# Optimization experiments

Measured on AMD Instinct MI355X. Metric: run time of the kernel, lower is better.

The kernel has to match this reference:

```python
import jax, jax.numpy as jnp
import numpy as np

N_HEADS = 4
N_HIDDEN = 64  # out_features // n_heads
NEG_SLOPE = 0.2


def setup_inputs() -> dict:
    key = jax.random.key(0)
    k1, k2, k3, k4, k5 = jax.random.split(key, 5)
    B, N, F_IN, F_OUT = 1, 4096, 128, 256
    h = jax.random.normal(k1, (B, N, F_IN), dtype=jnp.float32)
    adj_mat = jax.random.uniform(k2, (N, N, 1), dtype=jnp.float32)
    W_proj = jax.random.normal(k3, (F_IN, N_HEADS * N_HIDDEN), dtype=jnp.float32) / np.sqrt(F_IN)
    W_proj_attn = jax.random.normal(k4, (F_IN, N_HEADS * N_HIDDEN // 2), dtype=jnp.float32) / np.sqrt(F_IN)
    w_attn = jax.random.normal(k5, (N_HIDDEN,), dtype=jnp.float32) / np.sqrt(N_HIDDEN)
    return {"h": h, "adj_mat": adj_mat, "W_proj": W_proj, "W_proj_attn": W_proj_attn, "w_attn": w_attn}


def reference(h, adj_mat, W_proj, W_proj_attn, w_attn):
    B, N, _ = h.shape
    H, D = N_HEADS, N_HIDDEN
    half = D // 2
    # value projection: (B, N, H, D)
    g = (h @ W_proj).reshape(B, N, H, D)
    # attention-feature projection: (B, N, H, D//2)
    ga = (h @ W_proj_attn).reshape(B, N, H, half)
    # attn(cat([ga_i, ga_j])) decomposes linearly: e_ij = <w_l, ga_i> + <w_r, ga_j>
    # (identical math to the torch repeat/cat/Linear, without the NxNxD tensor)
    el = jnp.einsum('bnhk,k->bnh', ga, w_attn[:half])   # dest node i term
    er = jnp.einsum('bnhk,k->bnh', ga, w_attn[half:])   # source node j term
    e = jax.nn.leaky_relu(el[:, :, None, :] + er[:, None, :, :], NEG_SLOPE)  # (B, N, N, H)
    mask = adj_mat >= 0.5  # (N, N, 1) broadcasts over (B, N, N, H)
    e = jnp.where(mask, e, -jnp.inf)
    a = jax.nn.softmax(e, axis=2)  # softmax over source nodes j
    # dropout is identity in eval mode
    out = jnp.einsum('bijh,bjhf->bihf', a, g)  # (B, N, H, D)
    return out.reshape(B, N, H * D)  # is_concat=True
```

## Files before the change

### kernel.cpp

```cpp
#include <hip/hip_runtime.h>
#include <hip/hip_bf16.h>

typedef __bf16 bf16_t;
typedef __bf16 bf16x4 __attribute__((ext_vector_type(4)));
typedef __bf16 bf16x8 __attribute__((ext_vector_type(8)));
typedef float floatx4 __attribute__((ext_vector_type(4)));
typedef unsigned int u32;

#define N_NODES 4096
#define F_IN 128
#define NUM_HEADS 4
#define D_HID 64
#define F_OUT 256
#define NEG_SLOPE 0.2f
#define LOG2E 1.4426950408889634f
#define NWORDS 128

__global__ __launch_bounds__(256) void mask_kernel(
    const float* __restrict__ adj, u32* __restrict__ maskT)
{
    const int w = blockIdx.x * 256 + threadIdx.x;
    const float* src = adj + (size_t)w * 32;
    u32 bits = 0;
#pragma unroll
    for (int c = 0; c < 8; ++c) {
        const float4 v = *reinterpret_cast<const float4*>(src + c * 4);
        bits |= (u32)(v.x >= 0.5f) << (4 * c + 0);
        bits |= (u32)(v.y >= 0.5f) << (4 * c + 1);
        bits |= (u32)(v.z >= 0.5f) << (4 * c + 2);
        bits |= (u32)(v.w >= 0.5f) << (4 * c + 3);
    }
    const int row = w >> 7;
    const int jw  = w & 127;
    maskT[(size_t)jw * N_NODES + row] = bits;
}

__global__ __launch_bounds__(384) void proj_kernel(
    const float* __restrict__ hmat, const float* __restrict__ Wp,
    const float* __restrict__ Wa, const float* __restrict__ wattn,
    bf16_t* __restrict__ GB, float* __restrict__ el, float* __restrict__ er)
{
    const int t = threadIdx.x;
    const int j0 = blockIdx.x * 8;

    float acc[8] = {0.f, 0.f, 0.f, 0.f, 0.f, 0.f, 0.f, 0.f};

    const float* wptr;
    int stride;
    if (t < 256) { wptr = Wp + t;         stride = 256; }
    else         { wptr = Wa + (t - 256); stride = 128; }

    const float* hbase = hmat + (size_t)j0 * F_IN;

    for (int m = 0; m < F_IN; m += 4) {
        const float w0 = wptr[(size_t)(m + 0) * stride];
        const float w1 = wptr[(size_t)(m + 1) * stride];
        const float w2 = wptr[(size_t)(m + 2) * stride];
        const float w3 = wptr[(size_t)(m + 3) * stride];
#pragma unroll
        for (int jl = 0; jl < 8; ++jl) {
            const float4 hv = *reinterpret_cast<const float4*>(&hbase[jl * F_IN + m]);
            acc[jl] = fmaf(hv.w, w3, fmaf(hv.z, w2, fmaf(hv.y, w1, fmaf(hv.x, w0, acc[jl]))));
        }
    }

    if (t < 256) {
        const int h = t >> 6, f = t & 63;
        bf16x8 o;
#pragma unroll
        for (int q = 0; q < 8; ++q) o[q] = (bf16_t)acc[q];
        const size_t base = ((((size_t)h * 128 + (j0 >> 5)) * 4 + (f >> 4)) * 64
                             + (f & 15) + 16 * ((j0 >> 3) & 3)) * 8;
        *reinterpret_cast<bf16x8*>(&GB[base]) = o;
    } else {
        const int ta = t - 256;
        const int ha = ta >> 5, k = ta & 31;
        const float wl = wattn[k] * LOG2E, wr = wattn[32 + k] * LOG2E;
#pragma unroll
        for (int jl = 0; jl < 8; ++jl) {
            float vl = acc[jl] * wl;
            float vr = acc[jl] * wr;
#pragma unroll
            for (int s = 16; s >= 1; s >>= 1) {
                vl += __shfl_xor(vl, s, 64);
                vr += __shfl_xor(vr, s, 64);
            }
            if (k == 0) {
                el[ha * N_NODES + j0 + jl] = vl;
                er[ha * N_NODES + j0 + jl] = vr;
            }
        }
    }
}

__global__ __launch_bounds__(256, 4) void attn_kernel(
    const u32* __restrict__ maskT, const bf16_t* __restrict__ GB,
    const float* __restrict__ el, const float* __restrict__ er,
    float* __restrict__ numout, float* __restrict__ den_g,
    int ntiles)
{
    const int tid  = threadIdx.x;
    const int wave = tid >> 6;
    const int i0   = blockIdx.x * 128 + wave * 32;
    const int jc   = blockIdx.y;
    const int hh   = blockIdx.z;
    const int lane = tid & 63;
    const int m    = lane & 15;
    const int quad = lane >> 4;
    const int NS   = ntiles * 2;
    const int j32_0 = jc * NS;

    const float el_lo = el[hh * N_NODES + i0 + m];
    const float el_hi = el[hh * N_NODES + i0 + 16 + m];
    const u32*  mTp   = maskT + (size_t)j32_0 * N_NODES + i0 + m;
    const float* erp  = er + hh * N_NODES + j32_0 * 32 + quad * 8;
    const bf16_t* gb  = GB + (size_t)hh * (128 * 4 * 512)
                           + (size_t)j32_0 * 2048 + lane * 8;

    floatx4 accL0 = {0.f, 0.f, 0.f, 0.f};
    floatx4 accL1 = accL0, accL2 = accL0, accL3 = accL0;
    floatx4 accH0 = accL0, accH1 = accL0, accH2 = accL0, accH3 = accL0;
    float denL = 0.f, denH = 0.f;

    u32 mLc = mTp[0], mHc = mTp[16];
    float4 e0c = *reinterpret_cast<const float4*>(erp);
    float4 e1c = *reinterpret_cast<const float4*>(erp + 4);
    bf16x8 b0c = *reinterpret_cast<const bf16x8*>(gb);
    bf16x8 b1c = *reinterpret_cast<const bf16x8*>(gb + 512);
    bf16x8 b2c = *reinterpret_cast<const bf16x8*>(gb + 1024);
    bf16x8 b3c = *reinterpret_cast<const bf16x8*>(gb + 1536);

    for (int s = 0; s < NS; ++s) {
        const int d = (s + 1 < NS) ? 1 : 0;
        const u32    mLn = mTp[(size_t)d * N_NODES];
        const u32    mHn = mTp[(size_t)d * N_NODES + 16];
        const float4 e0n = *reinterpret_cast<const float4*>(erp + d * 32);
        const float4 e1n = *reinterpret_cast<const float4*>(erp + d * 32 + 4);
        const bf16_t* gpn = gb + (size_t)d * 2048;
        const bf16x8 b0n = *reinterpret_cast<const bf16x8*>(gpn);
        const bf16x8 b1n = *reinterpret_cast<const bf16x8*>(gpn + 512);
        const bf16x8 b2n = *reinterpret_cast<const bf16x8*>(gpn + 1024);
        const bf16x8 b3n = *reinterpret_cast<const bf16x8*>(gpn + 1536);

        const u32 byL = (mLc >> (quad * 8)) & 0xffu;
        const u32 byH = (mHc >> (quad * 8)) & 0xffu;
        const float ev[8] = {e0c.x, e0c.y, e0c.z, e0c.w, e1c.x, e1c.y, e1c.z, e1c.w};

        bf16x8 afL, afH;
        float dL = 0.f, dH = 0.f;
#pragma unroll
        for (int q = 0; q < 8; ++q) {
            float sL = el_lo + ev[q]; sL = fmaxf(sL, NEG_SLOPE * sL);
            float sH = el_hi + ev[q]; sH = fmaxf(sH, NEG_SLOPE * sH);
            const float pL = ((byL >> q) & 1u) ? __builtin_amdgcn_exp2f(sL) : 0.f;
            const float pH = ((byH >> q) & 1u) ? __builtin_amdgcn_exp2f(sH) : 0.f;
            dL += pL; dH += pH;
            afL[q] = (bf16_t)pL;
            afH[q] = (bf16_t)pH;
        }
        denL += dL; denH += dH;

        accL0 = __builtin_amdgcn_mfma_f32_16x16x32_bf16(afL, b0c, accL0, 0, 0, 0);
        accH0 = __builtin_amdgcn_mfma_f32_16x16x32_bf16(afH, b0c, accH0, 0, 0, 0);
        accL1 = __builtin_amdgcn_mfma_f32_16x16x32_bf16(afL, b1c, accL1, 0, 0, 0);
        accH1 = __builtin_amdgcn_mfma_f32_16x16x32_bf16(afH, b1c, accH1, 0, 0, 0);
        accL2 = __builtin_amdgcn_mfma_f32_16x16x32_bf16(afL, b2c, accL2, 0, 0, 0);
        accH2 = __builtin_amdgcn_mfma_f32_16x16x32_bf16(afH, b2c, accH2, 0, 0, 0);
        accL3 = __builtin_amdgcn_mfma_f32_16x16x32_bf16(afL, b3c, accL3, 0, 0, 0);
        accH3 = __builtin_amdgcn_mfma_f32_16x16x32_bf16(afH, b3c, accH3, 0, 0, 0);

        mLc = mLn; mHc = mHn; e0c = e0n; e1c = e1n;
        b0c = b0n; b1c = b1n; b2c = b2n; b3c = b3n;
        mTp += N_NODES;
        erp += 32;
        gb  += 2048;
    }

    denL += __shfl_xor(denL, 16, 64);
    denL += __shfl_xor(denL, 32, 64);
    denH += __shfl_xor(denH, 16, 64);
    denH += __shfl_xor(denH, 32, 64);

    float* nrow = numout + (size_t)jc * ((size_t)N_NODES * F_OUT);
    const int ibL = i0 + quad * 4;
    const int ibH = ibL + 16;
#pragma unroll
    for (int r = 0; r < 4; ++r) {
        float* dL = nrow + (size_t)(ibL + r) * F_OUT + hh * D_HID + m;
        dL[0]  = accL0[r];
        dL[16] = accL1[r];
        dL[32] = accL2[r];
        dL[48] = accL3[r];
        float* dH = nrow + (size_t)(ibH + r) * F_OUT + hh * D_HID + m;
        dH[0]  = accH0[r];
        dH[16] = accH1[r];
        dH[32] = accH2[r];
        dH[48] = accH3[r];
    }
    if (quad == 0) {
        den_g[((size_t)jc * N_NODES + i0 + m) * NUM_HEADS + hh] = denL;
        den_g[((size_t)jc * N_NODES + i0 + 16 + m) * NUM_HEADS + hh] = denH;
    }
}

template<int NJC>
__global__ __launch_bounds__(256) void reduce_kernel(
    const float* __restrict__ num, const float* __restrict__ den,
    float* __restrict__ out)
{
    const int t4   = blockIdx.x * 256 + threadIdx.x;
    const int base = t4 * 4;
    const int i  = base >> 8;
    const int hh = (base & 255) >> 6;
    float4 n = {0.f, 0.f, 0.f, 0.f};
    float d = 0.f;
#pragma unroll
    for (int jc = 0; jc < NJC; ++jc) {
        const float4 v = *reinterpret_cast<const float4*>(
            num + (size_t)jc * ((size_t)N_NODES * F_OUT) + base);
        n.x += v.x; n.y += v.y; n.z += v.z; n.w += v.w;
        d += den[((size_t)jc * N_NODES + i) * NUM_HEADS + hh];
    }
    const float rd = 1.0f / d;
    float4 o = {n.x * rd, n.y * rd, n.z * rd, n.w * rd};
    *reinterpret_cast<float4*>(out + base) = o;
}

extern "C" void kernel_launch(void* const* d_in, const int* in_sizes, int n_in,
                              void* d_out, int out_size, void* d_ws, size_t ws_size,
                              hipStream_t stream)
{
    const float* hmat = (const float*)d_in[0];
    const float* adj  = (const float*)d_in[1];
    const float* Wp   = (const float*)d_in[2];
    const float* Wa   = (const float*)d_in[3];
    const float* watt = (const float*)d_in[4];
    float* out = (float*)d_out;

    char* ws = (char*)d_ws;
    bf16_t* GB   = (bf16_t*)ws;
    float*  el   = (float*)(ws + (2ull << 20));
    float*  er   = (float*)(ws + (2ull << 20) + (64ull << 10));
    u32*    mskT = (u32*)(ws + (2ull << 20) + (128ull << 10));
    const size_t baseoff = (4ull << 20) + (128ull << 10);

    const size_t num_bytes = (size_t)N_NODES * F_OUT * 4;
    const size_t den_bytes = (size_t)N_NODES * NUM_HEADS * 4;
    const int njc = (ws_size >= baseoff + 8 * (num_bytes + den_bytes)) ? 8
                  : (ws_size >= baseoff + 4 * (num_bytes + den_bytes)) ? 4 : 2;

    float* num = (float*)(ws + baseoff);
    float* den = (float*)(ws + baseoff + (size_t)njc * num_bytes);

    proj_kernel<<<512, 384, 0, stream>>>(hmat, Wp, Wa, watt, GB, el, er);
    mask_kernel<<<(N_NODES * NWORDS) / 256, 256, 0, stream>>>(adj, mskT);
    attn_kernel<<<dim3(32, njc, NUM_HEADS), 256, 0, stream>>>(
        mskT, GB, el, er, num, den, (N_NODES / njc) / 64);
    if (njc == 8)      reduce_kernel<8><<<(N_NODES * F_OUT) / 1024, 256, 0, stream>>>(num, den, out);
    else if (njc == 4) reduce_kernel<4><<<(N_NODES * F_OUT) / 1024, 256, 0, stream>>>(num, den, out);
    else               reduce_kernel<2><<<(N_NODES * F_OUT) / 1024, 256, 0, stream>>>(num, den, out);
}
```

Measured before the change: 166.2 us.

## Fuse mask and projection kernels; compute softmax denominators via MFMA with ones

Merges the adjacency bit-packing kernel and the projection kernel into one launch, with the block index choosing which role a block plays. This removes one kernel launch and lets the two independent jobs run on the GPU at the same time. The attention loop now gets row sums by multiplying the bf16 probabilities by a ones vector on the matrix cores, which replaces the scalar float adds and cross-lane shuffles. It also packs the leaky-relu arithmetic into float2 vectors. The cost is two extra MFMAs per step, and the denominators are now summed from bf16-rounded probabilities, which slightly changes numerics.

```diff
diff --git a/kernel.cpp b/kernel.cpp
--- a/kernel.cpp
+++ b/kernel.cpp
@@ -4,6 +4,7 @@
 typedef __bf16 bf16_t;
 typedef __bf16 bf16x4 __attribute__((ext_vector_type(4)));
 typedef __bf16 bf16x8 __attribute__((ext_vector_type(8)));
+typedef float floatx2 __attribute__((ext_vector_type(2)));
 typedef float floatx4 __attribute__((ext_vector_type(4)));
 typedef unsigned int u32;
 
@@ -15,33 +16,36 @@
 #define NEG_SLOPE 0.2f
 #define LOG2E 1.4426950408889634f
 #define NWORDS 128
-
-__global__ __launch_bounds__(256) void mask_kernel(
-    const float* __restrict__ adj, u32* __restrict__ maskT)
-{
-    const int w = blockIdx.x * 256 + threadIdx.x;
-    const float* src = adj + (size_t)w * 32;
-    u32 bits = 0;
-#pragma unroll
-    for (int c = 0; c < 8; ++c) {
-        const float4 v = *reinterpret_cast<const float4*>(src + c * 4);
-        bits |= (u32)(v.x >= 0.5f) << (4 * c + 0);
-        bits |= (u32)(v.y >= 0.5f) << (4 * c + 1);
-        bits |= (u32)(v.z >= 0.5f) << (4 * c + 2);
-        bits |= (u32)(v.w >= 0.5f) << (4 * c + 3);
-    }
-    const int row = w >> 7;
-    const int jw  = w & 127;
-    maskT[(size_t)jw * N_NODES + row] = bits;
-}
-
-__global__ __launch_bounds__(384) void proj_kernel(
+#define MASK_BLOCKS 1366
+#define PROJ_BLOCKS 512
+
+__global__ __launch_bounds__(384) void prep_kernel(
+    const float* __restrict__ adj, u32* __restrict__ maskT,
     const float* __restrict__ hmat, const float* __restrict__ Wp,
     const float* __restrict__ Wa, const float* __restrict__ wattn,
     bf16_t* __restrict__ GB, float* __restrict__ el, float* __restrict__ er)
 {
-    const int t = threadIdx.x;
-    const int j0 = blockIdx.x * 8;
+    if (blockIdx.x < MASK_BLOCKS) {
+        const int w = blockIdx.x * 384 + threadIdx.x;
+        if (w < N_NODES * NWORDS) {
+            const float* src = adj + (size_t)w * 32;
+            u32 bits = 0;
+#pragma unroll
+            for (int c = 0; c < 8; ++c) {
+                const float4 v = *reinterpret_cast<const float4*>(src + c * 4);
+                bits |= (u32)(v.x >= 0.5f) << (4 * c + 0);
+                bits |= (u32)(v.y >= 0.5f) << (4 * c + 1);
+                bits |= (u32)(v.z >= 0.5f) << (4 * c + 2);
+                bits |= (u32)(v.w >= 0.5f) << (4 * c + 3);
+            }
+            const int row = w >> 7;
+            const int jw  = w & 127;
+            maskT[(size_t)jw * N_NODES + row] = bits;
+        }
+        return;
+    }
+    const int t  = threadIdx.x;
+    const int j0 = (blockIdx.x - MASK_BLOCKS) * 8;
 
     float acc[8] = {0.f, 0.f, 0.f, 0.f, 0.f, 0.f, 0.f, 0.f};
 
@@ -118,9 +122,11 @@
                            + (size_t)j32_0 * 2048 + lane * 8;
 
     floatx4 accL0 = {0.f, 0.f, 0.f, 0.f};
-    floatx4 accL1 = accL0, accL2 = accL0, accL3 = accL0;
-    floatx4 accH0 = accL0, accH1 = accL0, accH2 = accL0, accH3 = accL0;
-    float denL = 0.f, denH = 0.f;
+    floatx4 accL1 = accL0, accL2 = accL0, accL3 = accL0, accdL = accL0;
+    floatx4 accH0 = accL0, accH1 = accL0, accH2 = accL0, accH3 = accL0, accdH = accL0;
+    bf16x8 ones;
+#pragma unroll
+    for (int q = 0; q < 8; ++q) ones[q] = (bf16_t)1.0f;
 
     u32 mLc = mTp[0], mHc = mTp[16];
     float4 e0c = *reinterpret_cast<const float4*>(erp);
@@ -144,21 +150,30 @@
 
         const u32 byL = (mLc >> (quad * 8)) & 0xffu;
         const u32 byH = (mHc >> (quad * 8)) & 0xffu;
-        const float ev[8] = {e0c.x, e0c.y, e0c.z, e0c.w, e1c.x, e1c.y, e1c.z, e1c.w};
+        const floatx2 evp[4] = {{e0c.x, e0c.y}, {e0c.z, e0c.w},
+                                {e1c.x, e1c.y}, {e1c.z, e1c.w}};
+        const floatx2 eL2 = {el_lo, el_lo};
+        const floatx2 eH2 = {el_hi, el_hi};
 
         bf16x8 afL, afH;
-        float dL = 0.f, dH = 0.f;
-#pragma unroll
-        for (int q = 0; q < 8; ++q) {
-            float sL = el_lo + ev[q]; sL = fmaxf(sL, NEG_SLOPE * sL);
-            float sH = el_hi + ev[q]; sH = fmaxf(sH, NEG_SLOPE * sH);
-            const float pL = ((byL >> q) & 1u) ? __builtin_amdgcn_exp2f(sL) : 0.f;
-            const float pH = ((byH >> q) & 1u) ? __builtin_amdgcn_exp2f(sH) : 0.f;
-            dL += pL; dH += pH;
-            afL[q] = (bf16_t)pL;
-            afH[q] = (bf16_t)pH;
-        }
-        denL += dL; denH += dH;
+#pragma unroll
+        for (int qp = 0; qp < 4; ++qp) {
+            floatx2 sL = eL2 + evp[qp];
+            floatx2 sH = eH2 + evp[qp];
+            sL = __builtin_elementwise_max(sL, sL * NEG_SLOPE);
+            sH = __builtin_elementwise_max(sH, sH * NEG_SLOPE);
+            const float pL0 = ((byL >> (2 * qp))     & 1u) ? __builtin_amdgcn_exp2f(sL.x) : 0.f;
+            const float pL1 = ((byL >> (2 * qp + 1)) & 1u) ? __builtin_amdgcn_exp2f(sL.y) : 0.f;
+            const float pH0 = ((byH >> (2 * qp))     & 1u) ? __builtin_amdgcn_exp2f(sH.x) : 0.f;
+            const float pH1 = ((byH >> (2 * qp + 1)) & 1u) ? __builtin_amdgcn_exp2f(sH.y) : 0.f;
+            afL[2 * qp]     = (bf16_t)pL0;
+            afL[2 * qp + 1] = (bf16_t)pL1;
+            afH[2 * qp]     = (bf16_t)pH0;
+            afH[2 * qp + 1] = (bf16_t)pH1;
+        }
+
+        accdL = __builtin_amdgcn_mfma_f32_16x16x32_bf16(afL, ones, accdL, 0, 0, 0);
+        accdH = __builtin_amdgcn_mfma_f32_16x16x32_bf16(afH, ones, accdH, 0, 0, 0);
 
         accL0 = __builtin_amdgcn_mfma_f32_16x16x32_bf16(afL, b0c, accL0, 0, 0, 0);
         accH0 = __builtin_amdgcn_mfma_f32_16x16x32_bf16(afH, b0c, accH0, 0, 0, 0);
@@ -175,11 +190,6 @@
         erp += 32;
         gb  += 2048;
     }
-
-    denL += __shfl_xor(denL, 16, 64);
-    denL += __shfl_xor(denL, 32, 64);
-    denH += __shfl_xor(denH, 16, 64);
-    denH += __shfl_xor(denH, 32, 64);
 
     float* nrow = numout + (size_t)jc * ((size_t)N_NODES * F_OUT);
     const int ibL = i0 + quad * 4;
@@ -197,9 +207,12 @@
         dH[32] = accH2[r];
         dH[48] = accH3[r];
     }
-    if (quad == 0) {
-        den_g[((size_t)jc * N_NODES + i0 + m) * NUM_HEADS + hh] = denL;
-        den_g[((size_t)jc * N_NODES + i0 + 16 + m) * NUM_HEADS + hh] = denH;
+    if (m == 0) {
+#pragma unroll
+        for (int r = 0; r < 4; ++r) {
+            den_g[((size_t)jc * N_NODES + ibL + r) * NUM_HEADS + hh] = accdL[r];
+            den_g[((size_t)jc * N_NODES + ibH + r) * NUM_HEADS + hh] = accdH[r];
+        }
     }
 }
 
@@ -252,8 +265,8 @@
     float* num = (float*)(ws + baseoff);
     float* den = (float*)(ws + baseoff + (size_t)njc * num_bytes);
 
-    proj_kernel<<<512, 384, 0, stream>>>(hmat, Wp, Wa, watt, GB, el, er);
-    mask_kernel<<<(N_NODES * NWORDS) / 256, 256, 0, stream>>>(adj, mskT);
+    prep_kernel<<<MASK_BLOCKS + PROJ_BLOCKS, 384, 0, stream>>>(
+        adj, mskT, hmat, Wp, Wa, watt, GB, el, er);
     attn_kernel<<<dim3(32, njc, NUM_HEADS), 256, 0, stream>>>(
         mskT, GB, el, er, num, den, (N_NODES / njc) / 64);
     if (njc == 8)      reduce_kernel<8><<<(N_NODES * F_OUT) / 1024, 256, 0, stream>>>(num, den, out);
```

New measurement: 161.7 us. -2.7%, faster.
